# Performance work log

Measured on AMD Instinct MI355X. Metric: run time of the kernel, lower is better.

Reference implementation:

```python
import jax, jax.numpy as jnp
import numpy as np

ORDER = 7
MEMORY_DEPTH = 4
LAG_DEPTH = 2
B, S = 8, 65536


def _delay(sig, d):
    # prepend d zeros, drop last d samples (tf.concat-based delay in source)
    if d == 0:
        return sig
    return jnp.concatenate([jnp.zeros((d,), dtype=sig.dtype), sig[:-d]], axis=0)


def _setup_basis_matrix(x):
    # x: [N] complex64 -> [N, n_coeffs] complex64 (GMP basis)
    abs_x = jnp.abs(x)
    step = 2  # odd orders only (use_even=False)
    cols = []
    # main memory-polynomial terms: x * |x|^(k-1), delayed 0..M-1
    for order in range(1, ORDER + 1, step):
        branch = x * (abs_x ** (order - 1)).astype(x.dtype)
        for d in range(MEMORY_DEPTH):
            cols.append(_delay(branch, d))
    # lagging cross-terms: x * |x|^(k-1) shifted later by `lag`
    for order in range(3, ORDER + 1, step):
        abs_base = abs_x ** (order - 1)
        for lag in range(1, LAG_DEPTH + 1):
            lagged = jnp.concatenate(
                [jnp.zeros((lag,), dtype=abs_base.dtype), abs_base[:-lag]], axis=0)
            branch = x * lagged.astype(x.dtype)
            for d in range(MEMORY_DEPTH):
                cols.append(_delay(branch, d))
    # leading cross-terms: x * |x|^(k-1) shifted earlier by `lead`
    for order in range(3, ORDER + 1, step):
        abs_base = abs_x ** (order - 1)
        for lead in range(1, LAG_DEPTH + 1):
            led = jnp.concatenate(
                [abs_base[lead:], jnp.zeros((lead,), dtype=abs_base.dtype)], axis=0)
            branch = x * led.astype(x.dtype)
            for d in range(MEMORY_DEPTH):
                cols.append(_delay(branch, d))
    return jnp.stack(cols, axis=1)  # [N, 64]


def setup_inputs() -> dict:
    key = jax.random.key(0)
    k1, k2, k3, k4 = jax.random.split(key, 4)
    x_real = jax.random.normal(k1, (B, S), dtype=jnp.float32) * 0.3
    x_imag = jax.random.normal(k2, (B, S), dtype=jnp.float32) * 0.3
    # layer init is delta coeffs (coeffs[0]=1); use small random perturbation
    # around it so gradients are non-trivial
    coeffs_real = jax.random.normal(k3, (64, 1), dtype=jnp.float32) * 0.01
    coeffs_real = coeffs_real.at[0, 0].add(1.0)
    coeffs_imag = jax.random.normal(k4, (64, 1), dtype=jnp.float32) * 0.01
    return {"x_real": x_real, "x_imag": x_imag,
            "coeffs_real": coeffs_real, "coeffs_imag": coeffs_imag}


def reference(x_real, x_imag, coeffs_real, coeffs_imag):
    # predistort() on 2D input: flatten, build basis over the whole flat
    # signal, matmul with complex coeffs, reshape back to [B, S]
    x = (x_real + 1j * x_imag).reshape(-1).astype(jnp.complex64)  # [N]
    coeffs = (coeffs_real + 1j * coeffs_imag).astype(jnp.complex64)  # [64, 1]
    X = _setup_basis_matrix(x)  # [N, 64]
    y = (X @ coeffs).reshape(-1)  # [N]
    return y.reshape(x_real.shape)  # [B, S] complex64
```

## Files before the change

kernel.cpp:

```cpp
#include <hip/hip_runtime.h>


constexpr int BLOCK  = 256;
constexpr int HALO_L = 5;
constexpr int HALO_R = 2;
constexpr int TILE   = BLOCK + HALO_L + HALO_R;

__global__ __launch_bounds__(BLOCK) void dpd_gmp_kernel(
    const float* __restrict__ xr, const float* __restrict__ xi,
    const float* __restrict__ cr, const float* __restrict__ ci,
    float* __restrict__ out, int N, int out_size)
{
    __shared__ float sxr[TILE];
    __shared__ float sxi[TILE];

    const int tid  = threadIdx.x;
    const int base = blockIdx.x * BLOCK;

    for (int k = tid; k < TILE; k += BLOCK) {
        int m = base - HALO_L + k;
        bool ok = (m >= 0) && (m < N);
        sxr[k] = ok ? xr[m] : 0.0f;
        sxi[k] = ok ? xi[m] : 0.0f;
    }
    __syncthreads();

    const int n = base + tid;

    float wr[8], wi[8], p2[8], p4[8], p6[8];
#pragma unroll
    for (int w = 0; w < 8; ++w) {
        wr[w] = sxr[tid + w];
        wi[w] = sxi[tid + w];
        float s = wr[w] * wr[w] + wi[w] * wi[w];
        p2[w] = s;
        p4[w] = s * s;
        p6[w] = p4[w] * s;
    }

    float yr = 0.0f, yi = 0.0f;
#pragma unroll
    for (int d = 0; d < 4; ++d) {
        const int i = HALO_L - d;

        float Cr = cr[0 + d];
        float Ci = ci[0 + d];
        Cr = fmaf(cr[ 4 + d], p2[i],     Cr);  Ci = fmaf(ci[ 4 + d], p2[i],     Ci);
        Cr = fmaf(cr[ 8 + d], p4[i],     Cr);  Ci = fmaf(ci[ 8 + d], p4[i],     Ci);
        Cr = fmaf(cr[12 + d], p6[i],     Cr);  Ci = fmaf(ci[12 + d], p6[i],     Ci);
        Cr = fmaf(cr[16 + d], p2[i - 1], Cr);  Ci = fmaf(ci[16 + d], p2[i - 1], Ci);
        Cr = fmaf(cr[20 + d], p2[i - 2], Cr);  Ci = fmaf(ci[20 + d], p2[i - 2], Ci);
        Cr = fmaf(cr[24 + d], p4[i - 1], Cr);  Ci = fmaf(ci[24 + d], p4[i - 1], Ci);
        Cr = fmaf(cr[28 + d], p4[i - 2], Cr);  Ci = fmaf(ci[28 + d], p4[i - 2], Ci);
        Cr = fmaf(cr[32 + d], p6[i - 1], Cr);  Ci = fmaf(ci[32 + d], p6[i - 1], Ci);
        Cr = fmaf(cr[36 + d], p6[i - 2], Cr);  Ci = fmaf(ci[36 + d], p6[i - 2], Ci);
        Cr = fmaf(cr[40 + d], p2[i + 1], Cr);  Ci = fmaf(ci[40 + d], p2[i + 1], Ci);
        Cr = fmaf(cr[44 + d], p2[i + 2], Cr);  Ci = fmaf(ci[44 + d], p2[i + 2], Ci);
        Cr = fmaf(cr[48 + d], p4[i + 1], Cr);  Ci = fmaf(ci[48 + d], p4[i + 1], Ci);
        Cr = fmaf(cr[52 + d], p4[i + 2], Cr);  Ci = fmaf(ci[52 + d], p4[i + 2], Ci);
        Cr = fmaf(cr[56 + d], p6[i + 1], Cr);  Ci = fmaf(ci[56 + d], p6[i + 1], Ci);
        Cr = fmaf(cr[60 + d], p6[i + 2], Cr);  Ci = fmaf(ci[60 + d], p6[i + 2], Ci);

        yr = fmaf(wr[i],  Cr, yr);
        yr = fmaf(-wi[i], Ci, yr);
        yi = fmaf(wr[i],  Ci, yi);
        yi = fmaf(wi[i],  Cr, yi);
    }

    if (n < N) {
        if (n < out_size)     out[n]     = yr;
        if (N + n < out_size) out[N + n] = yi;
    }
}

extern "C" void kernel_launch(void* const* d_in, const int* in_sizes, int n_in,
                              void* d_out, int out_size, void* d_ws, size_t ws_size,
                              hipStream_t stream) {
    const float* xr = (const float*)d_in[0];
    const float* xi = (const float*)d_in[1];
    const float* cr = (const float*)d_in[2];
    const float* ci = (const float*)d_in[3];
    float* out = (float*)d_out;

    const int N = in_sizes[0];
    const int grid = (N + BLOCK - 1) / BLOCK;
    dpd_gmp_kernel<<<grid, BLOCK, 0, stream>>>(xr, xi, cr, ci, out, N, out_size);
}
```

Baseline: 64.40 us.

## Compute four outputs per thread with register windows and vectorized float4 I/O

Each thread now produces four consecutive outputs, loading a 16-sample window straight from global memory into registers with float4 loads instead of staging a tile in shared memory. The powers |x|^2, |x|^4 and |x|^6 are computed once per window and shared across the four outputs, and the coefficient loads are hoisted out of the per-output loop. Outputs are written with float4 stores. This drops the shared-memory staging and barrier and cuts redundant power and coefficient work, at the cost of higher register pressure, 4x fewer threads, and overlapping window reloads between neighbouring threads.

```diff
diff --git a/kernel.cpp b/kernel.cpp
--- a/kernel.cpp
+++ b/kernel.cpp
@@ -1,75 +1,111 @@
 #include <hip/hip_runtime.h>
 
 
-constexpr int BLOCK  = 256;
-constexpr int HALO_L = 5;
-constexpr int HALO_R = 2;
-constexpr int TILE   = BLOCK + HALO_L + HALO_R;
+constexpr int BLOCK = 256;
+constexpr int ITEMS = 4;
 
 __global__ __launch_bounds__(BLOCK) void dpd_gmp_kernel(
     const float* __restrict__ xr, const float* __restrict__ xi,
     const float* __restrict__ cr, const float* __restrict__ ci,
     float* __restrict__ out, int N, int out_size)
 {
-    __shared__ float sxr[TILE];
-    __shared__ float sxi[TILE];
+    const int gid = blockIdx.x * BLOCK + threadIdx.x;
+    const int n0  = gid * ITEMS;
+    if (n0 >= N) return;
 
-    const int tid  = threadIdx.x;
-    const int base = blockIdx.x * BLOCK;
-
-    for (int k = tid; k < TILE; k += BLOCK) {
-        int m = base - HALO_L + k;
-        bool ok = (m >= 0) && (m < N);
-        sxr[k] = ok ? xr[m] : 0.0f;
-        sxi[k] = ok ? xi[m] : 0.0f;
-    }
-    __syncthreads();
-
-    const int n = base + tid;
-
-    float wr[8], wi[8], p2[8], p4[8], p6[8];
+    float wr[16], wi[16];
+    const int m0 = n0 - 8;
+    if (m0 >= 0 && m0 + 16 <= N) {
+        const float4* r4 = reinterpret_cast<const float4*>(xr + m0);
+        const float4* i4 = reinterpret_cast<const float4*>(xi + m0);
 #pragma unroll
-    for (int w = 0; w < 8; ++w) {
-        wr[w] = sxr[tid + w];
-        wi[w] = sxi[tid + w];
-        float s = wr[w] * wr[w] + wi[w] * wi[w];
-        p2[w] = s;
-        p4[w] = s * s;
-        p6[w] = p4[w] * s;
+        for (int q = 0; q < 4; ++q) {
+            reinterpret_cast<float4*>(wr)[q] = r4[q];
+            reinterpret_cast<float4*>(wi)[q] = i4[q];
+        }
+    } else {
+#pragma unroll
+        for (int q = 0; q < 16; ++q) {
+            int m = m0 + q;
+            bool ok = (m >= 0) && (m < N);
+            wr[q] = ok ? xr[m] : 0.0f;
+            wi[q] = ok ? xi[m] : 0.0f;
+        }
     }
 
-    float yr = 0.0f, yi = 0.0f;
+    float p2[14], p4[14], p6[14];
+#pragma unroll
+    for (int q = 3; q <= 13; ++q) {
+        float s = wr[q] * wr[q] + wi[q] * wi[q];
+        p2[q] = s;
+        p4[q] = s * s;
+        p6[q] = p4[q] * s;
+    }
+
+    float yr[ITEMS] = {0.0f, 0.0f, 0.0f, 0.0f};
+    float yi[ITEMS] = {0.0f, 0.0f, 0.0f, 0.0f};
+
 #pragma unroll
     for (int d = 0; d < 4; ++d) {
-        const int i = HALO_L - d;
+        const float c0r  = cr[ 0 + d], c0i  = ci[ 0 + d];
+        const float c1r  = cr[ 4 + d], c1i  = ci[ 4 + d];
+        const float c2r  = cr[ 8 + d], c2i  = ci[ 8 + d];
+        const float c3r  = cr[12 + d], c3i  = ci[12 + d];
+        const float c4r  = cr[16 + d], c4i  = ci[16 + d];
+        const float c5r  = cr[20 + d], c5i  = ci[20 + d];
+        const float c6r  = cr[24 + d], c6i  = ci[24 + d];
+        const float c7r  = cr[28 + d], c7i  = ci[28 + d];
+        const float c8r  = cr[32 + d], c8i  = ci[32 + d];
+        const float c9r  = cr[36 + d], c9i  = ci[36 + d];
+        const float cAr  = cr[40 + d], cAi  = ci[40 + d];
+        const float cBr  = cr[44 + d], cBi  = ci[44 + d];
+        const float cCr  = cr[48 + d], cCi  = ci[48 + d];
+        const float cDr  = cr[52 + d], cDi  = ci[52 + d];
+        const float cEr  = cr[56 + d], cEi  = ci[56 + d];
+        const float cFr  = cr[60 + d], cFi  = ci[60 + d];
 
-        float Cr = cr[0 + d];
-        float Ci = ci[0 + d];
-        Cr = fmaf(cr[ 4 + d], p2[i],     Cr);  Ci = fmaf(ci[ 4 + d], p2[i],     Ci);
-        Cr = fmaf(cr[ 8 + d], p4[i],     Cr);  Ci = fmaf(ci[ 8 + d], p4[i],     Ci);
-        Cr = fmaf(cr[12 + d], p6[i],     Cr);  Ci = fmaf(ci[12 + d], p6[i],     Ci);
-        Cr = fmaf(cr[16 + d], p2[i - 1], Cr);  Ci = fmaf(ci[16 + d], p2[i - 1], Ci);
-        Cr = fmaf(cr[20 + d], p2[i - 2], Cr);  Ci = fmaf(ci[20 + d], p2[i - 2], Ci);
-        Cr = fmaf(cr[24 + d], p4[i - 1], Cr);  Ci = fmaf(ci[24 + d], p4[i - 1], Ci);
-        Cr = fmaf(cr[28 + d], p4[i - 2], Cr);  Ci = fmaf(ci[28 + d], p4[i - 2], Ci);
-        Cr = fmaf(cr[32 + d], p6[i - 1], Cr);  Ci = fmaf(ci[32 + d], p6[i - 1], Ci);
-        Cr = fmaf(cr[36 + d], p6[i - 2], Cr);  Ci = fmaf(ci[36 + d], p6[i - 2], Ci);
-        Cr = fmaf(cr[40 + d], p2[i + 1], Cr);  Ci = fmaf(ci[40 + d], p2[i + 1], Ci);
-        Cr = fmaf(cr[44 + d], p2[i + 2], Cr);  Ci = fmaf(ci[44 + d], p2[i + 2], Ci);
-        Cr = fmaf(cr[48 + d], p4[i + 1], Cr);  Ci = fmaf(ci[48 + d], p4[i + 1], Ci);
-        Cr = fmaf(cr[52 + d], p4[i + 2], Cr);  Ci = fmaf(ci[52 + d], p4[i + 2], Ci);
-        Cr = fmaf(cr[56 + d], p6[i + 1], Cr);  Ci = fmaf(ci[56 + d], p6[i + 1], Ci);
-        Cr = fmaf(cr[60 + d], p6[i + 2], Cr);  Ci = fmaf(ci[60 + d], p6[i + 2], Ci);
+#pragma unroll
+        for (int j = 0; j < ITEMS; ++j) {
+            const int i = 8 + j - d;
+            float Cr = c0r;
+            float Ci = c0i;
+            Cr = fmaf(c1r, p2[i],     Cr);  Ci = fmaf(c1i, p2[i],     Ci);
+            Cr = fmaf(c2r, p4[i],     Cr);  Ci = fmaf(c2i, p4[i],     Ci);
+            Cr = fmaf(c3r, p6[i],     Cr);  Ci = fmaf(c3i, p6[i],     Ci);
+            Cr = fmaf(c4r, p2[i - 1], Cr);  Ci = fmaf(c4i, p2[i - 1], Ci);
+            Cr = fmaf(c5r, p2[i - 2], Cr);  Ci = fmaf(c5i, p2[i - 2], Ci);
+            Cr = fmaf(c6r, p4[i - 1], Cr);  Ci = fmaf(c6i, p4[i - 1], Ci);
+            Cr = fmaf(c7r, p4[i - 2], Cr);  Ci = fmaf(c7i, p4[i - 2], Ci);
+            Cr = fmaf(c8r, p6[i - 1], Cr);  Ci = fmaf(c8i, p6[i - 1], Ci);
+            Cr = fmaf(c9r, p6[i - 2], Cr);  Ci = fmaf(c9i, p6[i - 2], Ci);
+            Cr = fmaf(cAr, p2[i + 1], Cr);  Ci = fmaf(cAi, p2[i + 1], Ci);
+            Cr = fmaf(cBr, p2[i + 2], Cr);  Ci = fmaf(cBi, p2[i + 2], Ci);
+            Cr = fmaf(cCr, p4[i + 1], Cr);  Ci = fmaf(cCi, p4[i + 1], Ci);
+            Cr = fmaf(cDr, p4[i + 2], Cr);  Ci = fmaf(cDi, p4[i + 2], Ci);
+            Cr = fmaf(cEr, p6[i + 1], Cr);  Ci = fmaf(cEi, p6[i + 1], Ci);
+            Cr = fmaf(cFr, p6[i + 2], Cr);  Ci = fmaf(cFi, p6[i + 2], Ci);
 
-        yr = fmaf(wr[i],  Cr, yr);
-        yr = fmaf(-wi[i], Ci, yr);
-        yi = fmaf(wr[i],  Ci, yi);
-        yi = fmaf(wi[i],  Cr, yi);
+            yr[j] = fmaf(wr[i],  Cr, yr[j]);
+            yr[j] = fmaf(-wi[i], Ci, yr[j]);
+            yi[j] = fmaf(wr[i],  Ci, yi[j]);
+            yi[j] = fmaf(wi[i],  Cr, yi[j]);
+        }
     }
 
-    if (n < N) {
-        if (n < out_size)     out[n]     = yr;
-        if (N + n < out_size) out[N + n] = yi;
+    if (n0 + ITEMS <= N && N + n0 + ITEMS <= out_size) {
+        *reinterpret_cast<float4*>(out + n0) =
+            make_float4(yr[0], yr[1], yr[2], yr[3]);
+        *reinterpret_cast<float4*>(out + N + n0) =
+            make_float4(yi[0], yi[1], yi[2], yi[3]);
+    } else {
+#pragma unroll
+        for (int j = 0; j < ITEMS; ++j) {
+            int n = n0 + j;
+            if (n < N) {
+                if (n < out_size)     out[n]     = yr[j];
+                if (N + n < out_size) out[N + n] = yi[j];
+            }
+        }
     }
 }
 
@@ -83,6 +119,7 @@
     float* out = (float*)d_out;
 
     const int N = in_sizes[0];
-    const int grid = (N + BLOCK - 1) / BLOCK;
+    const int elems_per_block = BLOCK * ITEMS;
+    const int grid = (N + elems_per_block - 1) / elems_per_block;
     dpd_gmp_kernel<<<grid, BLOCK, 0, stream>>>(xr, xi, cr, ci, out, N, out_size);
 }
```

After: 64.08 us. Within noise of the previous version (-0.5%).
